# Optimization experiments

Measured on AMD Instinct MI355X. Metric: run time of the kernel, lower is better.

## Reference

```python
import jax, jax.numpy as jnp
import numpy as np

B, S, D = 2, 2048, 2048
HQ, HK, HD = 16, 8, 128          # query heads, kv heads, head_dim
EPS = 1e-6
ROPE_THETA = 10000.0
SCALE = HD ** -0.5


def setup_inputs() -> dict:
    key = jax.random.key(0)
    ks = jax.random.split(key, 6)
    s = lambda fan_in: 1.0 / np.sqrt(fan_in)
    return {
        "hidden_states": jax.random.normal(ks[0], (B, S, D), jnp.float32),
        "positions": jnp.arange(S, dtype=jnp.int32),
        "Wq": jax.random.normal(ks[1], (D, HQ * HD), jnp.float32) * s(D),
        "Wk": jax.random.normal(ks[2], (D, HK * HD), jnp.float32) * s(D),
        "Wv": jax.random.normal(ks[3], (D, HK * HD), jnp.float32) * s(D),
        "Wo": jax.random.normal(ks[4], (HQ * HD, D), jnp.float32) * s(HQ * HD),
        "q_norm_w": jnp.ones((HD,), jnp.float32),
        "k_norm_w": jnp.ones((HD,), jnp.float32),
    }


def _rmsnorm(x, w):
    # RMSNorm over last (head_dim) axis, as in q_norm/k_norm
    var = jnp.mean(jnp.square(x), axis=-1, keepdims=True)
    return x * jax.lax.rsqrt(var + EPS) * w


def _rope(x, positions):
    # x: [B, S, H, HD]; rotate_half-style RoPE (Qwen3 convention)
    half = HD // 2
    inv_freq = 1.0 / (ROPE_THETA ** (jnp.arange(0, half, dtype=jnp.float32) / half))
    angles = positions.astype(jnp.float32)[:, None] * inv_freq[None, :]  # [S, half]
    cos = jnp.cos(angles)[None, :, None, :]  # [1, S, 1, half]
    sin = jnp.sin(angles)[None, :, None, :]
    x1, x2 = x[..., :half], x[..., half:]
    return jnp.concatenate([x1 * cos - x2 * sin, x2 * cos + x1 * sin], axis=-1)


def reference(hidden_states, positions, Wq, Wk, Wv, Wo, q_norm_w, k_norm_w):
    b, s, _ = hidden_states.shape
    q = (hidden_states @ Wq).reshape(b, s, HQ, HD)
    k = (hidden_states @ Wk).reshape(b, s, HK, HD)
    v = (hidden_states @ Wv).reshape(b, s, HK, HD)

    q = _rmsnorm(q, q_norm_w)
    k = _rmsnorm(k, k_norm_w)

    q = _rope(q, positions)
    k = _rope(k, positions)

    # GQA: repeat KV heads to match query heads
    groups = HQ // HK
    k = jnp.repeat(k, groups, axis=2)  # [B, S, HQ, HD]
    v = jnp.repeat(v, groups, axis=2)

    scores = jnp.einsum("bqhd,bkhd->bhqk", q, k) * SCALE  # [B, HQ, S, S]
    causal = jnp.tril(jnp.ones((s, s), dtype=bool))
    scores = jnp.where(causal[None, None], scores, jnp.float32(-jnp.inf))
    attn = jax.nn.softmax(scores, axis=-1)

    out = jnp.einsum("bhqk,bkhd->bqhd", attn, v).reshape(b, s, HQ * HD)
    return out @ Wo
```

## Files before the change

kernel.cpp:

```cpp
#include <hip/hip_runtime.h>
#include <cstdint>
#include <cstddef>

typedef _Float16 half8 __attribute__((ext_vector_type(8)));
typedef _Float16 half4 __attribute__((ext_vector_type(4)));
typedef float f32x4 __attribute__((ext_vector_type(4)));

#define DI __device__ __forceinline__

DI void gld_lds16(void* sp, const void* gp) {
  __builtin_amdgcn_global_load_lds(
      (const __attribute__((address_space(1))) void*)gp,
      (__attribute__((address_space(3))) void*)sp, 16, 0, 0);
}

__global__ __launch_bounds__(256) void cvt_f32_f16(const float* __restrict__ in,
                                                   _Float16* __restrict__ outp, int n8) {
  const int i = blockIdx.x * 256 + threadIdx.x;
  if (i >= n8) return;
  const float4* p = (const float4*)in + (size_t)i * 2;
  const float4 a = p[0], b = p[1];
  half8 h;
  h[0] = (_Float16)a.x; h[1] = (_Float16)a.y; h[2] = (_Float16)a.z; h[3] = (_Float16)a.w;
  h[4] = (_Float16)b.x; h[5] = (_Float16)b.y; h[6] = (_Float16)b.z; h[7] = (_Float16)b.w;
  *(half8*)(outp + (size_t)i * 8) = h;
}

__global__ __launch_bounds__(256) void transpose_cvt(const float* __restrict__ in,
                                                     _Float16* __restrict__ outp,
                                                     int R, int C) {
  __shared__ float t[32][33];
  const int tx = threadIdx.x & 31, ty = threadIdx.x >> 5;
  const int ctiles = C >> 5;
  const int tc = blockIdx.x % ctiles, tr = blockIdx.x / ctiles;
  const int r0 = tr * 32, c0 = tc * 32;
#pragma unroll
  for (int i = 0; i < 4; i++)
    t[ty + 8 * i][tx] = in[(size_t)(r0 + ty + 8 * i) * C + c0 + tx];
  __syncthreads();
#pragma unroll
  for (int i = 0; i < 4; i++) {
    const int rr = ty + 8 * i;
    outp[(size_t)(c0 + rr) * R + r0 + tx] = (_Float16)t[tx][rr];
  }
}

__global__ __launch_bounds__(256) void gemm_bt(const _Float16* __restrict__ A,
                                               const _Float16* __restrict__ Bt,
                                               float* __restrict__ C,
                                               int M, int N, int K) {
  __shared__ _Float16 sA[2][128 * 32];
  __shared__ _Float16 sB[2][128 * 32];
  const int tid = threadIdx.x;
  const int w = tid >> 6, l = tid & 63, lo = l & 15, hi = l >> 4;
  const int gx = gridDim.x, nwg = gx * gridDim.y;
  int bid = blockIdx.y * gx + blockIdx.x;
  bid = (bid & 7) * (nwg >> 3) + (bid >> 3);
  const int bn0 = (bid % gx) * 128, bm0 = (bid / gx) * 128;
  const int wm = w >> 1, wn = w & 1;
  const int srow = l >> 2;
  const int scol = (l & 3) * 8;

  f32x4 acc[4][4];
#pragma unroll
  for (int mi = 0; mi < 4; mi++)
#pragma unroll
    for (int ni = 0; ni < 4; ni++)
#pragma unroll
      for (int r = 0; r < 4; r++) acc[mi][ni][r] = 0.0f;

  auto stage = [&](int bi, int kt) {
#pragma unroll
    for (int i = 0; i < 2; ++i) {
      const int j = 2 * w + i;
      gld_lds16(&sA[bi][j * 512],
                A + (size_t)(bm0 + j * 16 + srow) * K + (size_t)kt * 32 + scol);
      gld_lds16(&sB[bi][j * 512],
                Bt + (size_t)(bn0 + j * 16 + srow) * K + (size_t)kt * 32 + scol);
    }
  };

  stage(0, 0);
  __syncthreads();
  const int KT = K >> 5;
#pragma unroll 1
  for (int kt = 0; kt < KT; ++kt) {
    const int cur = kt & 1;
    if (kt + 1 < KT) stage(cur ^ 1, kt + 1);
    half8 a[4], b[4];
#pragma unroll
    for (int mi = 0; mi < 4; mi++)
      a[mi] = *(const half8*)&sA[cur][(wm * 64 + mi * 16 + lo) * 32 + hi * 8];
#pragma unroll
    for (int ni = 0; ni < 4; ni++)
      b[ni] = *(const half8*)&sB[cur][(wn * 64 + ni * 16 + lo) * 32 + hi * 8];
#pragma unroll
    for (int mi = 0; mi < 4; mi++)
#pragma unroll
      for (int ni = 0; ni < 4; ni++)
        acc[mi][ni] = __builtin_amdgcn_mfma_f32_16x16x32_f16(a[mi], b[ni], acc[mi][ni], 0, 0, 0);
    __syncthreads();
  }

#pragma unroll
  for (int mi = 0; mi < 4; mi++)
#pragma unroll
    for (int ni = 0; ni < 4; ni++)
#pragma unroll
      for (int r = 0; r < 4; r++)
        C[(size_t)(bm0 + wm * 64 + mi * 16 + hi * 4 + r) * N +
          (bn0 + wn * 64 + ni * 16 + lo)] = acc[mi][ni][r];
}

__global__ __launch_bounds__(256) void norm_rope(const float* __restrict__ QKV,
                                                 const int* __restrict__ pos,
                                                 const float* __restrict__ qw,
                                                 const float* __restrict__ kw,
                                                 _Float16* __restrict__ Qb,
                                                 _Float16* __restrict__ Kb) {
  const int w = threadIdx.x >> 6, l = threadIdx.x & 63;
  const int wv = blockIdx.x * 4 + w;
  const int t = wv / 24, hh = wv - t * 24;
  const int b = t >> 11, s = t & 2047;
  const bool isq = hh < 16;
  const int col = isq ? hh * 128 : 2048 + (hh - 16) * 128;
  const float* x = QKV + (size_t)t * 4096 + col;
  const float x1 = x[l], x2 = x[l + 64];
  float ss = x1 * x1 + x2 * x2;
  ss += __shfl_xor(ss, 32); ss += __shfl_xor(ss, 16); ss += __shfl_xor(ss, 8);
  ss += __shfl_xor(ss, 4);  ss += __shfl_xor(ss, 2);  ss += __shfl_xor(ss, 1);
  const float rn = rsqrtf(ss * 0.0078125f + 1e-6f);
  const float* wt = isq ? qw : kw;
  const float n1 = x1 * rn * wt[l], n2 = x2 * rn * wt[l + 64];
  const float ang = (float)pos[s] * exp2f((float)l * -0.2076205059304601f);
  float sa, ca;
  sincosf(ang, &sa, &ca);
  const float qs = isq ? 0.12751731f : 1.0f;
  const float o1 = (n1 * ca - n2 * sa) * qs;
  const float o2 = (n2 * ca + n1 * sa) * qs;
  _Float16* dst = isq ? Qb + (((size_t)b * 16 + hh) * 2048 + s) * 128
                      : Kb + (((size_t)b * 8 + (hh - 16)) * 2048 + s) * 128;
  dst[l] = (_Float16)o1;
  dst[l + 64] = (_Float16)o2;
}

__global__ __launch_bounds__(256) void v_trans(const float* __restrict__ QKV,
                                               _Float16* __restrict__ Vt) {
  __shared__ float t[32][33];
  const int tx = threadIdx.x & 31, ty = threadIdx.x >> 5;
  const int dt = blockIdx.x & 3;
  const int st = (blockIdx.x >> 2) & 63;
  const int bh = blockIdx.x >> 8;
  const float* src = QKV + (size_t)((bh >> 3) * 2048 + st * 32) * 4096 +
                     3072 + (bh & 7) * 128 + dt * 32;
#pragma unroll
  for (int i = 0; i < 4; i++)
    t[ty + 8 * i][tx] = src[(size_t)(ty + 8 * i) * 4096 + tx];
  __syncthreads();
  _Float16* dst = Vt + ((size_t)bh * 128 + dt * 32) * 2048 + st * 32;
#pragma unroll
  for (int i = 0; i < 4; i++) {
    const int rr = ty + 8 * i;
    dst[(size_t)rr * 2048 + tx] = (_Float16)t[tx][rr];
  }
}

__global__ __launch_bounds__(256) void attn_fwd(const _Float16* __restrict__ Q,
                                                const _Float16* __restrict__ K,
                                                const _Float16* __restrict__ Vt,
                                                _Float16* __restrict__ AO) {
  __shared__ _Float16 sK[2][64 * 128];
  __shared__ _Float16 sV[2][128 * 64];
  __shared__ _Float16 P[4][16 * 80];
  const int tid = threadIdx.x, w = tid >> 6, l = tid & 63, lo = l & 15, hi = l >> 4;
  const int qt = 31 - (blockIdx.x >> 5);
  const int hq = blockIdx.x & 15;
  const int b = (blockIdx.x >> 4) & 1;
  const int hk = hq >> 1, q0 = qt * 64;
  const _Float16* Qh = Q + ((size_t)(b * 16 + hq) * 2048) * 128;
  const _Float16* Kh = K + ((size_t)(b * 8 + hk) * 2048) * 128;
  const _Float16* Vh = Vt + ((size_t)(b * 8 + hk) * 128) * 2048;
  const int qw0 = q0 + w * 16;

  auto stageK = [&](int bi, int kv0) {
#pragma unroll
    for (int i = 0; i < 4; ++i) {
      const int inst = w * 4 + i;
      const int r = inst * 4 + (l >> 4);
      const int cb = ((l & 15) * 16) ^ ((r & 7) << 4);
      gld_lds16(&sK[bi][inst * 512],
                (const char*)Kh + (size_t)(kv0 + r) * 256 + cb);
    }
  };
  auto stageV = [&](int bi, int kv0) {
#pragma unroll
    for (int i = 0; i < 4; ++i) {
      const int inst = w * 4 + i;
      const int r = inst * 8 + (l >> 3);
      const int cb = ((l & 7) * 16) ^ ((r & 7) << 4);
      gld_lds16(&sV[bi][inst * 512],
                (const char*)Vh + (size_t)r * 4096 + (size_t)kv0 * 2 + cb);
    }
  };

  half8 aq[4];
#pragma unroll
  for (int kc = 0; kc < 4; kc++)
    aq[kc] = *(const half8*)(Qh + (size_t)(qw0 + lo) * 128 + kc * 32 + hi * 8);

  f32x4 o[8];
#pragma unroll
  for (int dn = 0; dn < 8; dn++)
#pragma unroll
    for (int r = 0; r < 4; r++) o[dn][r] = 0.0f;
  float mrow = -1e30f, lrow = 0.0f;

  const int nt = qt + 1;
  stageK(0, 0);
  stageV(0, 0);
  __syncthreads();
#pragma unroll 1
  for (int kt = 0; kt < nt; ++kt) {
    const int kv0 = kt * 64;
    const int cur = kt & 1;
    if (kt + 1 < nt) {
      stageK(cur ^ 1, kv0 + 64);
      stageV(cur ^ 1, kv0 + 64);
    }
    const char* kb = (const char*)sK[cur];
    const char* vb = (const char*)sV[cur];
    f32x4 s[4];
#pragma unroll
    for (int ns = 0; ns < 4; ns++) {
#pragma unroll
      for (int r = 0; r < 4; r++) s[ns][r] = 0.0f;
      const int krow = ns * 16 + lo;
#pragma unroll
      for (int kc = 0; kc < 4; kc++) {
        half8 bk = *(const half8*)(kb + krow * 256 +
                                   ((kc * 64 + hi * 16) ^ ((krow & 7) << 4)));
        s[ns] = __builtin_amdgcn_mfma_f32_16x16x32_f16(bk, aq[kc], s[ns], 0, 0, 0);
      }
    }
    if (kt == nt - 1) {
#pragma unroll
      for (int ns = 0; ns < 4; ns++) {
        const int kv = kv0 + ns * 16 + hi * 4;
#pragma unroll
        for (int r = 0; r < 4; r++)
          if (kv + r > qw0 + lo) s[ns][r] = -1e30f;
      }
    }
    float tmax = s[0][0];
#pragma unroll
    for (int ns = 0; ns < 4; ns++)
#pragma unroll
      for (int r = 0; r < 4; r++) tmax = fmaxf(tmax, s[ns][r]);
    tmax = fmaxf(tmax, __shfl_xor(tmax, 16));
    tmax = fmaxf(tmax, __shfl_xor(tmax, 32));
    if (!__all(tmax <= mrow + 8.0f)) {
      const float mn = fmaxf(mrow, tmax);
      const float corr = exp2f(mrow - mn);
      mrow = mn;
      lrow *= corr;
      float c4[4];
#pragma unroll
      for (int r = 0; r < 4; r++) c4[r] = __shfl(corr, hi * 4 + r, 16);
#pragma unroll
      for (int dn = 0; dn < 8; dn++)
#pragma unroll
        for (int r = 0; r < 4; r++) o[dn][r] *= c4[r];
    }
    float psum = 0.0f;
#pragma unroll
    for (int ns = 0; ns < 4; ns++) {
      half4 pk;
#pragma unroll
      for (int r = 0; r < 4; r++) {
        const float p = exp2f(s[ns][r] - mrow);
        psum += p;
        pk[r] = (_Float16)p;
      }
      *(half4*)&P[w][lo * 80 + ns * 16 + hi * 4] = pk;
    }
    psum += __shfl_xor(psum, 16);
    psum += __shfl_xor(psum, 32);
    lrow += psum;
    asm volatile("s_waitcnt lgkmcnt(0)" ::: "memory");
    half8 ap0 = *(const half8*)&P[w][lo * 80 + hi * 8];
    half8 ap1 = *(const half8*)&P[w][lo * 80 + 32 + hi * 8];
#pragma unroll
    for (int dn = 0; dn < 8; dn++) {
      const int vrow = dn * 16 + lo;
      half8 bv0 = *(const half8*)(vb + vrow * 128 + ((hi * 16) ^ ((vrow & 7) << 4)));
      half8 bv1 = *(const half8*)(vb + vrow * 128 + ((64 + hi * 16) ^ ((vrow & 7) << 4)));
      o[dn] = __builtin_amdgcn_mfma_f32_16x16x32_f16(ap0, bv0, o[dn], 0, 0, 0);
      o[dn] = __builtin_amdgcn_mfma_f32_16x16x32_f16(ap1, bv1, o[dn], 0, 0, 0);
    }
    __syncthreads();
  }

  const float inv = 1.0f / lrow;
  float i4[4];
#pragma unroll
  for (int r = 0; r < 4; r++) i4[r] = __shfl(inv, hi * 4 + r, 16);
  const size_t tok = (size_t)b * 2048 + qw0;
#pragma unroll
  for (int dn = 0; dn < 8; dn++)
#pragma unroll
    for (int r = 0; r < 4; r++)
      AO[(tok + hi * 4 + r) * 2048 + hq * 128 + dn * 16 + lo] = (_Float16)(o[dn][r] * i4[r]);
}

extern "C" void kernel_launch(void* const* d_in, const int* in_sizes, int n_in,
                              void* d_out, int out_size, void* d_ws, size_t ws_size,
                              hipStream_t stream) {
  (void)in_sizes; (void)n_in; (void)out_size; (void)ws_size;
  const float* hs  = (const float*)d_in[0];
  const int*   pos = (const int*)d_in[1];
  const float* Wq  = (const float*)d_in[2];
  const float* Wk  = (const float*)d_in[3];
  const float* Wv  = (const float*)d_in[4];
  const float* Wo  = (const float*)d_in[5];
  const float* qnw = (const float*)d_in[6];
  const float* knw = (const float*)d_in[7];
  float* out = (float*)d_out;

  char* ws = (char*)d_ws;
  size_t off = 0;
  auto take = [&](size_t bytes) -> void* {
    void* p = ws + off;
    off += (bytes + 255) & ~(size_t)255;
    return p;
  };
  _Float16* Xh    = (_Float16*)take((size_t)4096 * 2048 * 2);
  _Float16* Wqkvt = (_Float16*)take((size_t)4096 * 2048 * 2);
  _Float16* Wot   = (_Float16*)take((size_t)2048 * 2048 * 2);
  float*    QKV   = (float*)take((size_t)4096 * 4096 * 4);
  _Float16* Qb    = (_Float16*)take((size_t)2 * 16 * 2048 * 128 * 2);
  _Float16* Kb    = (_Float16*)take((size_t)2 * 8 * 2048 * 128 * 2);
  _Float16* Vt    = (_Float16*)take((size_t)2 * 8 * 128 * 2048 * 2);
  _Float16* AO    = (_Float16*)take((size_t)4096 * 2048 * 2);

  cvt_f32_f16<<<4096, 256, 0, stream>>>(hs, Xh, 1048576);
  transpose_cvt<<<64 * 64, 256, 0, stream>>>(Wq, Wqkvt, 2048, 2048);
  transpose_cvt<<<64 * 32, 256, 0, stream>>>(Wk, Wqkvt + (size_t)2048 * 2048, 2048, 1024);
  transpose_cvt<<<64 * 32, 256, 0, stream>>>(Wv, Wqkvt + (size_t)3072 * 2048, 2048, 1024);
  transpose_cvt<<<64 * 64, 256, 0, stream>>>(Wo, Wot, 2048, 2048);
  gemm_bt<<<dim3(32, 32), 256, 0, stream>>>(Xh, Wqkvt, QKV, 4096, 4096, 2048);
  norm_rope<<<24576, 256, 0, stream>>>(QKV, pos, qnw, knw, Qb, Kb);
  v_trans<<<4096, 256, 0, stream>>>(QKV, Vt);
  attn_fwd<<<1024, 256, 0, stream>>>(Qb, Kb, Vt, AO);
  gemm_bt<<<dim3(16, 32), 256, 0, stream>>>(AO, Wot, out, 4096, 2048, 2048);
}
```

Before: 260.0 us.

## Replace GEMM with 8-wave, 4-stage pipelined, swizzled large-tile kernel

Replaces the 128x128 double-buffered 4-wave GEMM with a templated 512-thread kernel using 256x256 or 128x256 tiles. It uses a 4-deep LDS ring filled by direct global-to-LDS loads and XOR-swizzled LDS columns to avoid bank conflicts. Explicit vmcnt waits and s_setprio around the MFMA bursts let loads overlap compute. The larger tiles raise data reuse and launch exactly 256 workgroups for both projections, at the cost of much higher LDS use and register pressure, which caps occupancy.

After: 278.0 us. +7.0%, slower.

```diff
diff --git a/kernel.cpp b/kernel.cpp
--- a/kernel.cpp
+++ b/kernel.cpp
@@ -13,6 +13,9 @@
       (const __attribute__((address_space(1))) void*)gp,
       (__attribute__((address_space(3))) void*)sp, 16, 0, 0);
 }
+
+template <int N>
+DI void vmwait() { asm volatile("s_waitcnt vmcnt(%0)" :: "n"(N) : "memory"); }
 
 __global__ __launch_bounds__(256) void cvt_f32_f16(const float* __restrict__ in,
                                                    _Float16* __restrict__ outp, int n8) {
@@ -45,71 +48,114 @@
   }
 }
 
-__global__ __launch_bounds__(256) void gemm_bt(const _Float16* __restrict__ A,
-                                               const _Float16* __restrict__ Bt,
-                                               float* __restrict__ C,
-                                               int M, int N, int K) {
-  __shared__ _Float16 sA[2][128 * 32];
-  __shared__ _Float16 sB[2][128 * 32];
-  const int tid = threadIdx.x;
-  const int w = tid >> 6, l = tid & 63, lo = l & 15, hi = l >> 4;
-  const int gx = gridDim.x, nwg = gx * gridDim.y;
-  int bid = blockIdx.y * gx + blockIdx.x;
+template <int BM, int BN>
+__global__ __launch_bounds__(512, 2) void gemm8p(const _Float16* __restrict__ A,
+                                                 const _Float16* __restrict__ Bt,
+                                                 float* __restrict__ C,
+                                                 int N, int K) {
+  constexpr int MF = BM / 32;
+  constexpr int NF = BN / 64;
+  constexpr int MH = MF / 2;
+  constexpr int LA = BM / 128;
+  constexpr int LB = BN / 128;
+  constexpr int L = LA + LB;
+  __shared__ _Float16 sA[4][BM * 32];
+  __shared__ _Float16 sB[4][BN * 32];
+  const int tid = threadIdx.x, w = tid >> 6, l = tid & 63, lo = l & 15, hi = l >> 4;
+  const int wm = w >> 2, wn = w & 3;
+  const int nbn = N / BN;
+  const int nwg = gridDim.x;
+  int bid = blockIdx.x;
   bid = (bid & 7) * (nwg >> 3) + (bid >> 3);
-  const int bn0 = (bid % gx) * 128, bm0 = (bid / gx) * 128;
-  const int wm = w >> 1, wn = w & 1;
-  const int srow = l >> 2;
-  const int scol = (l & 3) * 8;
-
-  f32x4 acc[4][4];
-#pragma unroll
-  for (int mi = 0; mi < 4; mi++)
-#pragma unroll
-    for (int ni = 0; ni < 4; ni++)
-#pragma unroll
-      for (int r = 0; r < 4; r++) acc[mi][ni][r] = 0.0f;
-
-  auto stage = [&](int bi, int kt) {
-#pragma unroll
-    for (int i = 0; i < 2; ++i) {
-      const int j = 2 * w + i;
-      gld_lds16(&sA[bi][j * 512],
-                A + (size_t)(bm0 + j * 16 + srow) * K + (size_t)kt * 32 + scol);
-      gld_lds16(&sB[bi][j * 512],
-                Bt + (size_t)(bn0 + j * 16 + srow) * K + (size_t)kt * 32 + scol);
-    }
+  const int bm0 = (bid / nbn) * BM, bn0 = (bid % nbn) * BN;
+  const int kswz = (hi ^ ((lo >> 1) & 3)) * 8;
+  const int csel = ((l & 3) ^ ((l >> 3) & 3)) * 8;
+  const int NT = K >> 5;
+
+  size_t aoff[LA], boff[LB];
+#pragma unroll
+  for (int i = 0; i < LA; i++) {
+    const int r = (w * LA + i) * 16 + (l >> 2);
+    aoff[i] = (size_t)(bm0 + r) * K + csel;
+  }
+#pragma unroll
+  for (int i = 0; i < LB; i++) {
+    const int r = (w * LB + i) * 16 + (l >> 2);
+    boff[i] = (size_t)(bn0 + r) * K + csel;
+  }
+
+  auto stage = [&](int t) {
+    const int buf = t & 3;
+    const int kb = t * 32;
+#pragma unroll
+    for (int i = 0; i < LA; i++)
+      gld_lds16(&sA[buf][(w * LA + i) * 512], A + aoff[i] + kb);
+#pragma unroll
+    for (int i = 0; i < LB; i++)
+      gld_lds16(&sB[buf][(w * LB + i) * 512], Bt + boff[i] + kb);
   };
 
-  stage(0, 0);
-  __syncthreads();
-  const int KT = K >> 5;
+  f32x4 acc[MF][NF];
+#pragma unroll
+  for (int mf = 0; mf < MF; mf++)
+#pragma unroll
+    for (int nf = 0; nf < NF; nf++)
+#pragma unroll
+      for (int r = 0; r < 4; r++) acc[mf][nf][r] = 0.0f;
+
+  stage(0); stage(1); stage(2);
+  vmwait<2 * L>();
+  __builtin_amdgcn_s_barrier();
+
 #pragma unroll 1
-  for (int kt = 0; kt < KT; ++kt) {
-    const int cur = kt & 1;
-    if (kt + 1 < KT) stage(cur ^ 1, kt + 1);
-    half8 a[4], b[4];
-#pragma unroll
-    for (int mi = 0; mi < 4; mi++)
-      a[mi] = *(const half8*)&sA[cur][(wm * 64 + mi * 16 + lo) * 32 + hi * 8];
-#pragma unroll
-    for (int ni = 0; ni < 4; ni++)
-      b[ni] = *(const half8*)&sB[cur][(wn * 64 + ni * 16 + lo) * 32 + hi * 8];
-#pragma unroll
-    for (int mi = 0; mi < 4; mi++)
-#pragma unroll
-      for (int ni = 0; ni < 4; ni++)
-        acc[mi][ni] = __builtin_amdgcn_mfma_f32_16x16x32_f16(a[mi], b[ni], acc[mi][ni], 0, 0, 0);
-    __syncthreads();
-  }
-
-#pragma unroll
-  for (int mi = 0; mi < 4; mi++)
-#pragma unroll
-    for (int ni = 0; ni < 4; ni++)
+  for (int t = 0; t < NT; ++t) {
+    const int buf = t & 3;
+    if (t + 3 < NT) stage(t + 3);
+    half8 bfr[NF], afr[MH];
+#pragma unroll
+    for (int nf = 0; nf < NF; nf++)
+      bfr[nf] = *(const half8*)&sB[buf][(wn * NF * 16 + nf * 16 + lo) * 32 + kswz];
+#pragma unroll
+    for (int mf = 0; mf < MH; mf++)
+      afr[mf] = *(const half8*)&sA[buf][(wm * MF * 16 + mf * 16 + lo) * 32 + kswz];
+    __builtin_amdgcn_s_barrier();
+    __builtin_amdgcn_s_setprio(1);
+#pragma unroll
+    for (int mf = 0; mf < MH; mf++)
+#pragma unroll
+      for (int nf = 0; nf < NF; nf++)
+        acc[mf][nf] =
+            __builtin_amdgcn_mfma_f32_16x16x32_f16(afr[mf], bfr[nf], acc[mf][nf], 0, 0, 0);
+    __builtin_amdgcn_s_setprio(0);
+    __builtin_amdgcn_s_barrier();
+    half8 afr1[MH];
+#pragma unroll
+    for (int mf = 0; mf < MH; mf++)
+      afr1[mf] =
+          *(const half8*)&sA[buf][(wm * MF * 16 + (MH + mf) * 16 + lo) * 32 + kswz];
+    __builtin_amdgcn_s_barrier();
+    __builtin_amdgcn_s_setprio(1);
+#pragma unroll
+    for (int mf = 0; mf < MH; mf++)
+#pragma unroll
+      for (int nf = 0; nf < NF; nf++)
+        acc[MH + mf][nf] = __builtin_amdgcn_mfma_f32_16x16x32_f16(afr1[mf], bfr[nf],
+                                                                  acc[MH + mf][nf], 0, 0, 0);
+    __builtin_amdgcn_s_setprio(0);
+    if (t < NT - 3) vmwait<2 * L>();
+    else if (t == NT - 3) vmwait<L>();
+    else if (t == NT - 2) vmwait<0>();
+    __builtin_amdgcn_s_barrier();
+  }
+
+#pragma unroll
+  for (int mf = 0; mf < MF; mf++)
+#pragma unroll
+    for (int nf = 0; nf < NF; nf++)
 #pragma unroll
       for (int r = 0; r < 4; r++)
-        C[(size_t)(bm0 + wm * 64 + mi * 16 + hi * 4 + r) * N +
-          (bn0 + wn * 64 + ni * 16 + lo)] = acc[mi][ni][r];
+        C[(size_t)(bm0 + wm * MF * 16 + mf * 16 + hi * 4 + r) * N +
+          (bn0 + wn * NF * 16 + nf * 16 + lo)] = acc[mf][nf][r];
 }
 
 __global__ __launch_bounds__(256) void norm_rope(const float* __restrict__ QKV,
@@ -347,9 +393,9 @@
   transpose_cvt<<<64 * 32, 256, 0, stream>>>(Wk, Wqkvt + (size_t)2048 * 2048, 2048, 1024);
   transpose_cvt<<<64 * 32, 256, 0, stream>>>(Wv, Wqkvt + (size_t)3072 * 2048, 2048, 1024);
   transpose_cvt<<<64 * 64, 256, 0, stream>>>(Wo, Wot, 2048, 2048);
-  gemm_bt<<<dim3(32, 32), 256, 0, stream>>>(Xh, Wqkvt, QKV, 4096, 4096, 2048);
+  gemm8p<256, 256><<<256, 512, 0, stream>>>(Xh, Wqkvt, QKV, 4096, 2048);
   norm_rope<<<24576, 256, 0, stream>>>(QKV, pos, qnw, knw, Qb, Kb);
   v_trans<<<4096, 256, 0, stream>>>(QKV, Vt);
   attn_fwd<<<1024, 256, 0, stream>>>(Qb, Kb, Vt, AO);
-  gemm_bt<<<dim3(16, 32), 256, 0, stream>>>(AO, Wot, out, 4096, 2048, 2048);
-}
+  gemm8p<128, 256><<<256, 512, 0, stream>>>(AO, Wot, out, 2048, 2048);
+}
```
